# Performance work log

Hardware: AMD Instinct MI355X
Metric: run time of the kernel (lower is better)

## Reference

```python
import jax, jax.numpy as jnp
import numpy as np

B, T, V_ENC, V_DEC, E, H, A, MAX_SEQ = 32, 128, 32000, 32000, 512, 1024, 1024, 100


def setup_inputs() -> dict:
    key = jax.random.key(0)
    ks = jax.random.split(key, 16)
    s = 0.05
    p = lambda k, shape: jax.random.normal(k, shape, dtype=jnp.float32) * s
    inputs = jax.random.randint(ks[0], (B, T), 0, V_ENC, dtype=jnp.int32)
    return {
        'inputs': inputs,
        'enc_emb': p(ks[1], (V_ENC, E)),
        'enc_Wih': p(ks[2], (3 * H, E)),
        'enc_Whh': p(ks[3], (3 * H, H)),
        'enc_bih': p(ks[4], (3 * H,)),
        'enc_bhh': p(ks[5], (3 * H,)),
        'dec_emb': p(ks[6], (V_DEC, E)).at[0].set(0.0),  # padding_idx=0
        'dec_Wih': p(ks[7], (3 * H, E + A)),
        'dec_Whh': p(ks[8], (3 * H, H)),
        'dec_bih': p(ks[9], (3 * H,)),
        'dec_bhh': p(ks[10], (3 * H,)),
        'attn_W': p(ks[11], (A, 2 * H)),
        'attn_b': p(ks[12], (A,)),
        'cls_W': p(ks[13], (V_DEC, A)),
        'cls_b': p(ks[14], (V_DEC,)),
    }


def _gru_cell(x, h, Wih, Whh, bih, bhh):
    # PyTorch GRU cell math
    gi = x @ Wih.T + bih
    gh = h @ Whh.T + bhh
    i_r, i_z, i_n = jnp.split(gi, 3, axis=-1)
    h_r, h_z, h_n = jnp.split(gh, 3, axis=-1)
    r = jax.nn.sigmoid(i_r + h_r)
    z = jax.nn.sigmoid(i_z + h_z)
    n = jnp.tanh(i_n + r * h_n)
    return (1.0 - z) * n + z * h


def reference(inputs, enc_emb, enc_Wih, enc_Whh, enc_bih, enc_bhh,
              dec_emb, dec_Wih, dec_Whh, dec_bih, dec_bhh,
              attn_W, attn_b, cls_W, cls_b):
    b = inputs.shape[0]
    # ----- encoder -----
    emb = enc_emb[inputs]  # [B,T,E]
    def enc_step(h, x_t):
        h2 = _gru_cell(x_t, h, enc_Wih, enc_Whh, enc_bih, enc_bhh)
        return h2, h2
    h0 = jnp.zeros((b, H), emb.dtype)
    h_enc, enc_outputs = jax.lax.scan(enc_step, h0, emb.transpose(1, 0, 2))
    enc_outputs = enc_outputs.transpose(1, 0, 2)  # [B,T,H]

    # ----- greedy decoder, fixed max_sequence=100 steps -----
    def dec_step(carry, _):
        ids, attn_vec, h = carry
        x = jnp.concatenate([dec_emb[ids], attn_vec], axis=1)  # [B,E+A]
        h2 = _gru_cell(x, h, dec_Wih, dec_Whh, dec_bih, dec_bhh)  # [B,H]
        score = jnp.einsum('bth,bh->bt', enc_outputs, h2)
        w = jax.nn.softmax(score, axis=1)  # [B,T]
        context = jnp.einsum('bt,bth->bh', w, enc_outputs)  # [B,H]
        av = jnp.tanh(jnp.concatenate([context, h2], axis=1) @ attn_W.T + attn_b)  # [B,A]
        preds = av @ cls_W.T + cls_b  # [B,V]
        nids = jnp.argmax(preds, axis=1).astype(jnp.int32)
        return (nids, av, h2), (preds, w)

    carry0 = (jnp.zeros((b,), jnp.int32), jnp.zeros((b, A), jnp.float32), h_enc)
    _, (predictions, attn_weights) = jax.lax.scan(dec_step, carry0, None, length=MAX_SEQ)
    return predictions, attn_weights  # [100,B,V], [100,B,T]
```

## Files before the change

### kernel.cpp

```cpp
#include <hip/hip_runtime.h>
#include <hip/hip_cooperative_groups.h>
#include <math.h>

namespace cg = cooperative_groups;

#define NBLK 256
#define NTHR 1024
#define AG  __HIP_MEMORY_SCOPE_AGENT
#define SYS __HIP_MEMORY_SCOPE_SYSTEM

typedef float f4v __attribute__((ext_vector_type(4)));

constexpr int Bc = 32, Tc = 128, Ec = 512, Hc = 1024, Ac = 1024, Vc = 32000, Sc = 100;
constexpr long long OUT_ATTN = (long long)Sc * Bc * Vc;

constexpr long long O_ENCWIH = 0;
constexpr long long O_ENCWHH = O_ENCWIH + (long long)512 * 3072;
constexpr long long O_DECWIH = O_ENCWHH + (long long)1024 * 3072;
constexpr long long O_DECWHH = O_DECWIH + (long long)1536 * 3072;
constexpr long long O_ATTNWT = O_DECWHH + (long long)1024 * 3072;
constexpr long long O_CLSWT  = O_ATTNWT + (long long)2048 * 1024;
constexpr long long O_XENCT  = O_CLSWT + (long long)1024 * 32000;
constexpr long long O_GI     = O_XENCT + (long long)128 * 512 * 32;
constexpr long long O_ENCOUT = O_GI + (long long)128 * 32 * 3072;
constexpr long long O_H0     = O_ENCOUT + (long long)32 * 128 * 1024;
constexpr long long O_H1     = O_H0 + 32768;
constexpr long long O_H2     = O_H1 + 32768;
constexpr long long O_AVT    = O_H2 + 32768;
constexpr long long O_CTXT   = O_AVT + 32768;
constexpr long long O_PADEC  = O_CTXT + 32768;
constexpr long long O_PAENC  = O_PADEC + (long long)10 * 32 * 4096;
constexpr long long O_PAC    = O_PAENC + (long long)8 * 32 * 3072;
constexpr long long O_PARGV  = O_PAC + (long long)16 * 32 * 1024;
constexpr long long O_PARGI  = O_PARGV + 8000;
constexpr long long O_CNT    = O_PARGI + 8000;
constexpr long long WS_FLOATS = O_CNT + 1024;

#define CI_DA  0
#define CI_DB  32
#define CI_FIN 64
#define CI_DD  96
#define CI_H   128
#define CI_ENC 160
#define CI_DC  480

__device__ __forceinline__ float cohL(const float* p) { return __hip_atomic_load(p, __ATOMIC_RELAXED, SYS); }
__device__ __forceinline__ int   cohLi(const int* p) { return __hip_atomic_load(p, __ATOMIC_RELAXED, SYS); }

__device__ __forceinline__ void spinw(int* c, int tgt, int tid) {
  if (tid == 0) {
    while (__hip_atomic_load(c, __ATOMIC_RELAXED, AG) < tgt)
      __builtin_amdgcn_s_sleep(4);
  }
  __syncthreads();
}
__device__ __forceinline__ void sigp(int* c, int tid) {
  __syncthreads();
  if (tid == 0) {
    __builtin_amdgcn_fence(__ATOMIC_RELEASE, "agent");
    atomicAdd(c, 1);
  }
}

__global__ __launch_bounds__(NTHR, 4) void seq2seq_kernel(
    const int* __restrict__ inp, const float* __restrict__ encEmb,
    const float* __restrict__ encWih, const float* __restrict__ encWhh,
    const float* __restrict__ encBih, const float* __restrict__ encBhh,
    const float* __restrict__ decEmb, const float* __restrict__ decWih,
    const float* __restrict__ decWhh, const float* __restrict__ decBih,
    const float* __restrict__ decBhh, const float* __restrict__ attnW,
    const float* __restrict__ attnB, const float* __restrict__ clsW,
    const float* __restrict__ clsB, float* __restrict__ out,
    float* __restrict__ ws)
{
  cg::grid_group grid = cg::this_grid();
  const int bid = blockIdx.x, tid = threadIdx.x;
  const long long gtid = (long long)bid * NTHR + tid;
  int* cnt = (int*)(ws + O_CNT);

  __shared__ float smem[10624];
  int* sflag = (int*)(smem + 10600);
  int* nids  = (int*)(smem + 10368);

  {
    const int sg = tid >> 8, st = tid & 255;
    float* tile = smem + sg * 1056;
    const int c = st & 31, rr = st >> 5;
    for (int it = 0; it < 46; ++it) {
      int job = it * (NBLK * 4) + bid * 4 + sg;
      const float* src = nullptr; float* dst = nullptr;
      int R = 0, C = 0, tr = 0, tcd = 0;
      bool valid = true;
      int j = job;
      if (j < 1536)               { src = encWih; dst = ws + O_ENCWIH; R = 3072;  C = 512;  tr = j >> 4; tcd = j & 15; }
      else if ((j -= 1536) < 3072){ src = encWhh; dst = ws + O_ENCWHH; R = 3072;  C = 1024; tr = j >> 5; tcd = j & 31; }
      else if ((j -= 3072) < 4608){ src = decWih; dst = ws + O_DECWIH; R = 3072;  C = 1536; tr = j / 48; tcd = j % 48; }
      else if ((j -= 4608) < 3072){ src = decWhh; dst = ws + O_DECWHH; R = 3072;  C = 1024; tr = j >> 5; tcd = j & 31; }
      else if ((j -= 3072) < 2048){ src = attnW;  dst = ws + O_ATTNWT; R = 1024;  C = 2048; tr = j >> 6; tcd = j & 63; }
      else if ((j -= 2048) < 32000){src = clsW;   dst = ws + O_CLSWT;  R = 32000; C = 1024; tr = j >> 5; tcd = j & 31; }
      else valid = false;
      if (valid) {
        #pragma unroll
        for (int i = 0; i < 4; ++i) {
          int r = rr + (i << 3);
          tile[r * 33 + c] = src[(long long)(tr * 32 + r) * C + tcd * 32 + c];
        }
      }
      __syncthreads();
      if (valid) {
        #pragma unroll
        for (int i = 0; i < 4; ++i) {
          int c2 = rr + (i << 3);
          dst[(long long)(tcd * 32 + c2) * R + tr * 32 + c] = tile[c * 33 + c2];
        }
      }
      __syncthreads();
    }
  }
  for (long long i = gtid; i < (long long)128 * 512 * 32; i += (long long)NBLK * NTHR) {
    int b = (int)(i & 31);
    int k = (int)((i >> 5) & 511);
    int t = (int)(i >> 14);
    int row = inp[b * Tc + t];
    ws[O_XENCT + i] = encEmb[(long long)row * Ec + k];
  }
  for (long long i = gtid; i < 32768; i += (long long)NBLK * NTHR) {
    ws[O_H0 + i] = 0.f;
    ws[O_AVT + i] = 0.f;
  }
  grid.sync();

  for (int it = 0; it < 6; ++it) {
    int job = it * NBLK + bid;
    int t = job / 12, jc = job % 12;
    int jl = tid & 255, bq = tid >> 8;
    int j = jc * 256 + jl;
    float acc[8] = {0,0,0,0,0,0,0,0};
    const float* xb = ws + O_XENCT + (long long)t * 512 * 32 + bq * 8;
    const float* wb = ws + O_ENCWIH + j;
    for (int k = 0; k < 512; ++k) {
      float w = wb[(long long)k * 3072];
      float4 x0 = *(const float4*)(xb + k * 32);
      float4 x1 = *(const float4*)(xb + k * 32 + 4);
      acc[0] += x0.x * w; acc[1] += x0.y * w; acc[2] += x0.z * w; acc[3] += x0.w * w;
      acc[4] += x1.x * w; acc[5] += x1.y * w; acc[6] += x1.z * w; acc[7] += x1.w * w;
    }
    float bias = encBih[j];
    #pragma unroll
    for (int i = 0; i < 8; ++i) {
      int b = bq * 8 + i;
      __builtin_nontemporal_store(acc[i] + bias, &ws[O_GI + ((long long)t * 32 + b) * 3072 + j]);
    }
  }
  grid.sync();

  if (bid < 192) {
    int g = bid / 64, rem = bid % 64;
    int jc = rem >> 3, kp = rem & 7;
    for (int t = 0; t < Tc; ++t) {
      long long RD = (t & 1) ? O_H1 : O_H0;
      long long WR = (t & 1) ? O_H0 : O_H1;
      spinw(cnt + CI_H, 8 * t, tid);
      {
        const float* hsrc = ws + RD + kp * 4096;
        #pragma unroll
        for (int r = 0; r < 4; ++r)
          smem[r * 1024 + tid] = cohL(hsrc + r * 1024 + tid);
      }
      __syncthreads();
      int jl = tid & 127, bq = tid >> 7;
      int col = g * 1024 + jc * 128 + jl;
      int b0 = bq * 4;
      float acc[4] = {0,0,0,0};
      const float* hb = smem + b0;
      const float* wb = ws + O_ENCWHH + (long long)(kp * 128) * 3072 + col;
      for (int k = 0; k < 128; ++k) {
        float w = wb[(long long)k * 3072];
        float4 x = *(const float4*)(hb + k * 32);
        acc[0] += x.x * w; acc[1] += x.y * w; acc[2] += x.z * w; acc[3] += x.w * w;
      }
      #pragma unroll
      for (int i = 0; i < 4; ++i)
        ws[O_PAENC + ((long long)(kp * 32) + b0 + i) * 3072 + col] = acc[i];
      __syncthreads();
      if (tid == 0) {
        __builtin_amdgcn_fence(__ATOMIC_RELEASE, "agent");
        int old = atomicAdd(cnt + CI_ENC + jc * 32, 1);
        *sflag = (old == 24 * (t + 1) - 1) ? 1 : 0;
      }
      __syncthreads();
      if (*sflag) {
        int fj = tid & 127, fq = tid >> 7;
        int j = jc * 128 + fj;
        #pragma unroll
        for (int i = 0; i < 4; ++i) {
          int b = fq * 4 + i;
          float gr = 0, gz = 0, gn = 0;
          #pragma unroll
          for (int kp2 = 0; kp2 < 8; ++kp2) {
            long long base = O_PAENC + ((long long)(kp2 * 32) + b) * 3072;
            gr += cohL(&ws[base + j]);
            gz += cohL(&ws[base + 1024 + j]);
            gn += cohL(&ws[base + 2048 + j]);
          }
          long long gib = O_GI + ((long long)t * 32 + b) * 3072;
          float gir = ws[gib + j], giz = ws[gib + 1024 + j], gin = ws[gib + 2048 + j];
          float r = 1.f / (1.f + expf(-(gir + gr + encBhh[j])));
          float z = 1.f / (1.f + expf(-(giz + gz + encBhh[1024 + j])));
          float n = tanhf(gin + r * (gn + encBhh[2048 + j]));
          float hold = cohL(&ws[RD + (long long)j * 32 + b]);
          float hn = (1.f - z) * n + z * hold;
          ws[WR + (long long)j * 32 + b] = hn;
          ws[O_ENCOUT + ((long long)b * 128 + t) * 1024 + j] = hn;
          if (t == Tc - 1) ws[O_H2 + (long long)j * 32 + b] = hn;
        }
        sigp(cnt + CI_H, tid);
      }
      __syncthreads();
    }
  }

  for (int s = 0; s < Sc; ++s) {
    if (bid < 240) {
      int gate, loc;
      if (bid < 80)       { gate = 0; loc = bid; }
      else if (bid < 160) { gate = 1; loc = bid - 80; }
      else if (bid < 208) { gate = 2; loc = bid - 160; }
      else                { gate = 3; loc = bid - 208; }
      int nkp = (gate < 2) ? 10 : ((gate == 2) ? 6 : 4);
      int jc = loc / nkp, kp = loc % nkp;
      int kg = (gate == 3 ? 1536 : 0) + kp * 256;
      bool embp = (kg < 512);
      if (s == 0) {
        spinw(cnt + CI_H, 8 * Tc, tid);
        if (tid < 32) nids[tid] = 0;
        __syncthreads();
      } else if (embp) {
        spinw(cnt + CI_DD, 250 * s, tid);
        float* pv = smem; int* pi = (int*)(smem + 1024);
        int b = tid & 31, ch = tid >> 5;
        float bv = -3.4e38f; int bi = 0;
        for (int r = ch; r < 250; r += 32) {
          float v = cohL(&ws[O_PARGV + r * 32 + b]);
          int ix = cohLi(((int*)(ws + O_PARGI)) + r * 32 + b);
          if (v > bv || (v == bv && ix < bi)) { bv = v; bi = ix; }
        }
        pv[ch * 32 + b] = bv; pi[ch * 32 + b] = bi;
        __syncthreads();
        if (tid < 32) {
          float bb = -3.4e38f; int bbi = 0;
          for (int c2 = 0; c2 < 32; ++c2) {
            float v = pv[c2 * 32 + tid]; int ix = pi[c2 * 32 + tid];
            if (v > bb || (v == bb && ix < bbi)) { bb = v; bbi = ix; }
          }
          nids[tid] = bbi;
        }
        __syncthreads();
      } else {
        spinw(cnt + CI_DB, 32 * s, tid);
        spinw(cnt + CI_FIN, 16 * s, tid);
      }
      int jl = tid & 127, bq = tid >> 7;
      int b0 = bq * 4;
      int jcol = jc * 128 + jl;
      int wcol = (gate >= 2 ? 2048 : gate * 1024) + jcol;
      const float* wb = (kg < 1536) ? (ws + O_DECWIH + (long long)kg * 3072 + wcol)
                                    : (ws + O_DECWHH + (long long)(kg - 1536) * 3072 + wcol);
      float acc[4] = {0,0,0,0};
      if (embp) {
        const float* e0 = decEmb + (long long)nids[b0    ] * 512 + kg;
        const float* e1 = decEmb + (long long)nids[b0 + 1] * 512 + kg;
        const float* e2 = decEmb + (long long)nids[b0 + 2] * 512 + kg;
        const float* e3 = decEmb + (long long)nids[b0 + 3] * 512 + kg;
        for (int k = 0; k < 256; ++k) {
          float w = wb[(long long)k * 3072];
          acc[0] += e0[k] * w; acc[1] += e1[k] * w; acc[2] += e2[k] * w; acc[3] += e3[k] * w;
        }
      } else {
        const float* src = (kg < 1536) ? (ws + O_AVT + (long long)(kg - 512) * 32)
                                       : (ws + O_H2 + (long long)(kg - 1536) * 32);
        #pragma unroll
        for (int r = 0; r < 8; ++r)
          smem[r * 1024 + tid] = cohL(src + r * 1024 + tid);
        __syncthreads();
        const float* xb = smem + b0;
        for (int k = 0; k < 256; ++k) {
          float w = wb[(long long)k * 3072];
          float4 x = *(const float4*)(xb + k * 32);
          acc[0] += x.x * w; acc[1] += x.y * w; acc[2] += x.z * w; acc[3] += x.w * w;
        }
      }
      int colout = gate * 1024 + jcol;
      #pragma unroll
      for (int i = 0; i < 4; ++i)
        ws[O_PADEC + ((long long)(kp * 32) + b0 + i) * 4096 + colout] = acc[i];
      sigp(cnt + CI_DA, tid);
    }

    if (bid < 32) {
      spinw(cnt + CI_DA, 240 * (s + 1), tid);
      int b = bid;
      float* h2l = smem;
      float* scl = smem + 1024;
      float* wl  = smem + 1152;
      float* red = smem + 1280;
      {
        int j = tid;
        float gr = 0, gz = 0, gin = 0, ghn = 0;
        #pragma unroll
        for (int kp = 0; kp < 10; ++kp) {
          long long base = O_PADEC + ((long long)(kp * 32) + b) * 4096;
          gr += cohL(&ws[base + j]);
          gz += cohL(&ws[base + 1024 + j]);
          if (kp < 6) gin += cohL(&ws[base + 2048 + j]);
          if (kp < 4) ghn += cohL(&ws[base + 3072 + j]);
        }
        float r = 1.f / (1.f + expf(-(gr + decBih[j] + decBhh[j])));
        float z = 1.f / (1.f + expf(-(gz + decBih[1024 + j] + decBhh[1024 + j])));
        float n = tanhf(gin + decBih[2048 + j] + r * (ghn + decBhh[2048 + j]));
        float hold = ws[O_H2 + (long long)j * 32 + b];
        float h2 = (1.f - z) * n + z * hold;
        ws[O_H2 + (long long)j * 32 + b] = h2;
        h2l[j] = h2;
      }
      __syncthreads();
      {
        int wv = tid >> 6, lane = tid & 63;
        float h2v[16];
        #pragma unroll
        for (int i = 0; i < 16; ++i) h2v[i] = h2l[lane + (i << 6)];
        for (int t8 = 0; t8 < 8; ++t8) {
          int tt = wv * 8 + t8;
          const float* eo = ws + O_ENCOUT + ((long long)b * 128 + tt) * 1024 + lane;
          float a = 0;
          #pragma unroll
          for (int i = 0; i < 16; ++i) a += eo[i << 6] * h2v[i];
          #pragma unroll
          for (int off = 32; off; off >>= 1) a += __shfl_xor(a, off, 64);
          if (lane == 0) scl[tt] = a;
        }
      }
      __syncthreads();
      {
        float v = 0, m = -3.4e38f;
        if (tid < 128) {
          v = scl[tid]; m = v;
          #pragma unroll
          for (int off = 32; off; off >>= 1) m = fmaxf(m, __shfl_xor(m, off, 64));
          if ((tid & 63) == 0) red[tid >> 6] = m;
        }
        __syncthreads();
        float mm = fmaxf(red[0], red[1]);
        float e = 0.f;
        if (tid < 128) {
          e = expf(v - mm);
          float se = e;
          #pragma unroll
          for (int off = 32; off; off >>= 1) se += __shfl_xor(se, off, 64);
          if ((tid & 63) == 0) red[2 + (tid >> 6)] = se;
        }
        __syncthreads();
        if (tid < 128) {
          float wgt = e / (red[2] + red[3]);
          wl[tid] = wgt;
          __builtin_nontemporal_store(wgt, &out[OUT_ATTN + ((long long)s * 32 + b) * 128 + tid]);
        }
      }
      __syncthreads();
      {
        int j = tid;
        float a = 0;
        const float* eo = ws + O_ENCOUT + (long long)b * 128 * 1024 + j;
        for (int tt = 0; tt < 128; ++tt) a += wl[tt] * eo[(long long)tt * 1024];
        ws[O_CTXT + (long long)j * 32 + b] = a;
      }
      sigp(cnt + CI_DB, tid);
    }

    {
      spinw(cnt + CI_DB, 32 * (s + 1), tid);
      int jc = bid >> 4, kp = bid & 15;
      int kk0 = kp * 128;
      {
        const float* src = (kk0 < 1024) ? (ws + O_CTXT + (long long)kk0 * 32)
                                        : (ws + O_H2 + (long long)(kk0 - 1024) * 32);
        #pragma unroll
        for (int r = 0; r < 4; ++r)
          smem[r * 1024 + tid] = cohL(src + r * 1024 + tid);
      }
      __syncthreads();
      int jl = tid & 63, bh = tid >> 6;
      int b0 = bh * 2;
      int j = jc * 64 + jl;
      float acc0 = 0, acc1 = 0;
      const float* wb = ws + O_ATTNWT + (long long)kk0 * 1024 + j;
      const float* xb = smem + b0;
      for (int k = 0; k < 128; ++k) {
        float w = wb[(long long)k * 1024];
        float2 x = *(const float2*)(xb + k * 32);
        acc0 += x.x * w; acc1 += x.y * w;
      }
      ws[O_PAC + ((long long)(kp * 32) + b0) * 1024 + j] = acc0;
      ws[O_PAC + ((long long)(kp * 32) + b0 + 1) * 1024 + j] = acc1;
      __syncthreads();
      if (tid == 0) {
        __builtin_amdgcn_fence(__ATOMIC_RELEASE, "agent");
        int old = atomicAdd(cnt + CI_DC + jc * 32, 1);
        *sflag = (old == 16 * (s + 1) - 1) ? 1 : 0;
      }
      __syncthreads();
      if (*sflag) {
        #pragma unroll
        for (int o = 0; o < 2; ++o) {
          int oo = tid + o * 1024;
          int j2 = jc * 64 + (oo >> 5), b = oo & 31;
          float sum = 0;
          #pragma unroll
          for (int kp2 = 0; kp2 < 16; ++kp2)
            sum += cohL(&ws[O_PAC + ((long long)(kp2 * 32) + b) * 1024 + j2]);
          ws[O_AVT + (long long)j2 * 32 + b] = tanhf(sum + attnB[j2]);
        }
        sigp(cnt + CI_FIN, tid);
      }
      __syncthreads();
    }

    if (bid < 250) {
      spinw(cnt + CI_FIN, 16 * (s + 1), tid);
      float* wc  = smem;
      float* sav = smem + 8192;
      int jl = tid & 127, bg = tid >> 7;
      int b0 = bg * 4;
      int j = bid * 128 + jl;
      float acc[4] = {0,0,0,0};
      for (int kc = 0; kc < 1024; kc += 64) {
        #pragma unroll
        for (int i = 0; i < 2; ++i) {
          int t4 = tid + i * 1024;
          int kk = t4 >> 5, c4 = t4 & 31;
          f4v wv = __builtin_nontemporal_load(
            (const f4v*)(ws + O_CLSWT + (long long)(kc + kk) * 32000 + bid * 128 + c4 * 4));
          *(f4v*)(wc + kk * 128 + c4 * 4) = wv;
        }
        #pragma unroll
        for (int i = 0; i < 2; ++i)
          sav[i * 1024 + tid] = cohL(ws + O_AVT + (long long)kc * 32 + i * 1024 + tid);
        __syncthreads();
        for (int k = 0; k < 64; ++k) {
          float w = wc[k * 128 + jl];
          float4 a = *(const float4*)(sav + k * 32 + b0);
          acc[0] += a.x * w; acc[1] += a.y * w; acc[2] += a.z * w; acc[3] += a.w * w;
        }
        __syncthreads();
      }
      float cb = clsB[j];
      float pvv[4];
      #pragma unroll
      for (int i = 0; i < 4; ++i) {
        pvv[i] = acc[i] + cb;
        __builtin_nontemporal_store(pvv[i], &out[((long long)s * 32 + b0 + i) * 32000 + j]);
      }
      float* lv = smem;
      int*   li = (int*)(smem + 4096);
      __syncthreads();
      #pragma unroll
      for (int i = 0; i < 4; ++i) {
        lv[(b0 + i) * 128 + jl] = pvv[i];
        li[(b0 + i) * 128 + jl] = j;
      }
      __syncthreads();
      float* l2v = smem + 8192;
      int*   l2i = (int*)(smem + 9216);
      {
        int b = tid >> 5, r = tid & 31;
        float bv = -3.4e38f; int bi2 = 0;
        #pragma unroll
        for (int i = 0; i < 4; ++i) {
          float v = lv[b * 128 + r + (i << 5)];
          int ix = li[b * 128 + r + (i << 5)];
          if (v > bv || (v == bv && ix < bi2)) { bv = v; bi2 = ix; }
        }
        l2v[b * 32 + r] = bv; l2i[b * 32 + r] = bi2;
      }
      __syncthreads();
      if (tid < 32) {
        float bv = -3.4e38f; int bi2 = 0;
        for (int r = 0; r < 32; ++r) {
          float v = l2v[tid * 32 + r]; int ix = l2i[tid * 32 + r];
          if (v > bv || (v == bv && ix < bi2)) { bv = v; bi2 = ix; }
        }
        ws[O_PARGV + bid * 32 + tid] = bv;
        ((int*)(ws + O_PARGI))[bid * 32 + tid] = bi2;
      }
      sigp(cnt + CI_DD, tid);
    }
  }
}

extern "C" void kernel_launch(void* const* d_in, const int* in_sizes, int n_in,
                              void* d_out, int out_size, void* d_ws, size_t ws_size,
                              hipStream_t stream) {
  const int*   inp    = (const int*)  d_in[0];
  const float* encEmb = (const float*)d_in[1];
  const float* encWih = (const float*)d_in[2];
  const float* encWhh = (const float*)d_in[3];
  const float* encBih = (const float*)d_in[4];
  const float* encBhh = (const float*)d_in[5];
  const float* decEmb = (const float*)d_in[6];
  const float* decWih = (const float*)d_in[7];
  const float* decWhh = (const float*)d_in[8];
  const float* decBih = (const float*)d_in[9];
  const float* decBhh = (const float*)d_in[10];
  const float* attnW  = (const float*)d_in[11];
  const float* attnB  = (const float*)d_in[12];
  const float* clsW   = (const float*)d_in[13];
  const float* clsB   = (const float*)d_in[14];
  float* out = (float*)d_out;
  float* ws  = (float*)d_ws;

  if (ws_size < (size_t)WS_FLOATS * sizeof(float)) return;

  (void)hipMemsetAsync(ws + O_CNT, 0, 1024 * sizeof(int), stream);

  void* args[] = { &inp, &encEmb, &encWih, &encWhh, &encBih, &encBhh,
                   &decEmb, &decWih, &decWhh, &decBih, &decBhh,
                   &attnW, &attnB, &clsW, &clsB, &out, &ws };
  (void)hipLaunchCooperativeKernel((void*)seq2seq_kernel, dim3(NBLK), dim3(NTHR),
                                   args, 0, stream);
}
```

Baseline: 46.03 ms.

## Replace atomic counters with per-block flag slots and restructure attention projection

Swaps the shared atomic counters used for inter-stage barriers in the decoder loop for per-block flag slots holding step tags. Waiters poll many slots in parallel, one thread per producer, which removes atomic contention on a single counter. The attention output projection moves from a 256-block split-K with partial sums and last-arriver reduction to 32 blocks that each compute full dot products, dropping one sync round and the partial buffer at the cost of less parallelism. The class-weight loads also become ordinary loads instead of nontemporal ones.

```diff
diff --git a/kernel.cpp b/kernel.cpp
--- a/kernel.cpp
+++ b/kernel.cpp
@@ -30,19 +30,19 @@
 constexpr long long O_CTXT   = O_AVT + 32768;
 constexpr long long O_PADEC  = O_CTXT + 32768;
 constexpr long long O_PAENC  = O_PADEC + (long long)10 * 32 * 4096;
-constexpr long long O_PAC    = O_PAENC + (long long)8 * 32 * 3072;
-constexpr long long O_PARGV  = O_PAC + (long long)16 * 32 * 1024;
+constexpr long long O_PARGV  = O_PAENC + (long long)8 * 32 * 3072;
 constexpr long long O_PARGI  = O_PARGV + 8000;
 constexpr long long O_CNT    = O_PARGI + 8000;
-constexpr long long WS_FLOATS = O_CNT + 1024;
-
-#define CI_DA  0
-#define CI_DB  32
-#define CI_FIN 64
-#define CI_DD  96
+constexpr long long O_SLOT   = O_CNT + 1024;
+constexpr long long WS_FLOATS = O_SLOT + 1024;
+
 #define CI_H   128
 #define CI_ENC 160
-#define CI_DC  480
+
+#define SL_DA  0
+#define SL_DB  256
+#define SL_FIN 320
+#define SL_DD  384
 
 __device__ __forceinline__ float cohL(const float* p) { return __hip_atomic_load(p, __ATOMIC_RELAXED, SYS); }
 __device__ __forceinline__ int   cohLi(const int* p) { return __hip_atomic_load(p, __ATOMIC_RELAXED, SYS); }
@@ -60,6 +60,21 @@
     __builtin_amdgcn_fence(__ATOMIC_RELEASE, "agent");
     atomicAdd(c, 1);
   }
+}
+
+__device__ __forceinline__ void sigs(int* slotp, int tag, int tid) {
+  __syncthreads();
+  if (tid == 0) {
+    __builtin_amdgcn_fence(__ATOMIC_RELEASE, "agent");
+    __hip_atomic_store(slotp, tag, __ATOMIC_RELAXED, AG);
+  }
+}
+__device__ __forceinline__ void pollN(const int* slots, int n, int tag, int tid) {
+  if (tid < n) {
+    while (__hip_atomic_load(&slots[tid], __ATOMIC_RELAXED, AG) < tag)
+      __builtin_amdgcn_s_sleep(2);
+  }
+  __syncthreads();
 }
 
 __global__ __launch_bounds__(NTHR, 4) void seq2seq_kernel(
@@ -76,7 +91,8 @@
   cg::grid_group grid = cg::this_grid();
   const int bid = blockIdx.x, tid = threadIdx.x;
   const long long gtid = (long long)bid * NTHR + tid;
-  int* cnt = (int*)(ws + O_CNT);
+  int* cnt  = (int*)(ws + O_CNT);
+  int* slot = (int*)(ws + O_SLOT);
 
   __shared__ float smem[10624];
   int* sflag = (int*)(smem + 10600);
@@ -236,7 +252,7 @@
         if (tid < 32) nids[tid] = 0;
         __syncthreads();
       } else if (embp) {
-        spinw(cnt + CI_DD, 250 * s, tid);
+        pollN(slot + SL_DD, 250, s, tid);
         float* pv = smem; int* pi = (int*)(smem + 1024);
         int b = tid & 31, ch = tid >> 5;
         float bv = -3.4e38f; int bi = 0;
@@ -256,9 +272,10 @@
           nids[tid] = bbi;
         }
         __syncthreads();
+      } else if (kg >= 1536) {
+        pollN(slot + SL_DB, 32, s, tid);
       } else {
-        spinw(cnt + CI_DB, 32 * s, tid);
-        spinw(cnt + CI_FIN, 16 * s, tid);
+        pollN(slot + SL_FIN, 32, s, tid);
       }
       int jl = tid & 127, bq = tid >> 7;
       int b0 = bq * 4;
@@ -294,11 +311,11 @@
       #pragma unroll
       for (int i = 0; i < 4; ++i)
         ws[O_PADEC + ((long long)(kp * 32) + b0 + i) * 4096 + colout] = acc[i];
-      sigp(cnt + CI_DA, tid);
+      sigs(slot + SL_DA + bid, s + 1, tid);
     }
 
     if (bid < 32) {
-      spinw(cnt + CI_DA, 240 * (s + 1), tid);
+      pollN(slot + SL_DA, 240, s + 1, tid);
       int b = bid;
       float* h2l = smem;
       float* scl = smem + 1024;
@@ -374,59 +391,36 @@
         for (int tt = 0; tt < 128; ++tt) a += wl[tt] * eo[(long long)tt * 1024];
         ws[O_CTXT + (long long)j * 32 + b] = a;
       }
-      sigp(cnt + CI_DB, tid);
-    }
-
-    {
-      spinw(cnt + CI_DB, 32 * (s + 1), tid);
-      int jc = bid >> 4, kp = bid & 15;
-      int kk0 = kp * 128;
-      {
+      sigs(slot + SL_DB + bid, s + 1, tid);
+    }
+
+    if (bid < 32) {
+      pollN(slot + SL_DB, 32, s + 1, tid);
+      int jf = tid >> 5, b = tid & 31;
+      int j = (bid << 5) + jf;
+      float sum = 0.f;
+      #pragma unroll 1
+      for (int kp = 0; kp < 16; ++kp) {
+        int kk0 = kp * 128;
         const float* src = (kk0 < 1024) ? (ws + O_CTXT + (long long)kk0 * 32)
                                         : (ws + O_H2 + (long long)(kk0 - 1024) * 32);
         #pragma unroll
         for (int r = 0; r < 4; ++r)
           smem[r * 1024 + tid] = cohL(src + r * 1024 + tid);
-      }
-      __syncthreads();
-      int jl = tid & 63, bh = tid >> 6;
-      int b0 = bh * 2;
-      int j = jc * 64 + jl;
-      float acc0 = 0, acc1 = 0;
-      const float* wb = ws + O_ATTNWT + (long long)kk0 * 1024 + j;
-      const float* xb = smem + b0;
-      for (int k = 0; k < 128; ++k) {
-        float w = wb[(long long)k * 1024];
-        float2 x = *(const float2*)(xb + k * 32);
-        acc0 += x.x * w; acc1 += x.y * w;
-      }
-      ws[O_PAC + ((long long)(kp * 32) + b0) * 1024 + j] = acc0;
-      ws[O_PAC + ((long long)(kp * 32) + b0 + 1) * 1024 + j] = acc1;
-      __syncthreads();
-      if (tid == 0) {
-        __builtin_amdgcn_fence(__ATOMIC_RELEASE, "agent");
-        int old = atomicAdd(cnt + CI_DC + jc * 32, 1);
-        *sflag = (old == 16 * (s + 1) - 1) ? 1 : 0;
-      }
-      __syncthreads();
-      if (*sflag) {
-        #pragma unroll
-        for (int o = 0; o < 2; ++o) {
-          int oo = tid + o * 1024;
-          int j2 = jc * 64 + (oo >> 5), b = oo & 31;
-          float sum = 0;
-          #pragma unroll
-          for (int kp2 = 0; kp2 < 16; ++kp2)
-            sum += cohL(&ws[O_PAC + ((long long)(kp2 * 32) + b) * 1024 + j2]);
-          ws[O_AVT + (long long)j2 * 32 + b] = tanhf(sum + attnB[j2]);
-        }
-        sigp(cnt + CI_FIN, tid);
-      }
-      __syncthreads();
+        __syncthreads();
+        const float* wk = ws + O_ATTNWT + (long long)kk0 * 1024 + j;
+        float pp = 0.f;
+        for (int k = 0; k < 128; ++k)
+          pp += smem[k * 32 + b] * wk[(long long)k * 1024];
+        sum += pp;
+        __syncthreads();
+      }
+      ws[O_AVT + (long long)j * 32 + b] = tanhf(sum + attnB[j]);
+      sigs(slot + SL_FIN + bid, s + 1, tid);
     }
 
     if (bid < 250) {
-      spinw(cnt + CI_FIN, 16 * (s + 1), tid);
+      pollN(slot + SL_FIN, 32, s + 1, tid);
       float* wc  = smem;
       float* sav = smem + 8192;
       int jl = tid & 127, bg = tid >> 7;
@@ -438,9 +432,8 @@
         for (int i = 0; i < 2; ++i) {
           int t4 = tid + i * 1024;
           int kk = t4 >> 5, c4 = t4 & 31;
-          f4v wv = __builtin_nontemporal_load(
-            (const f4v*)(ws + O_CLSWT + (long long)(kc + kk) * 32000 + bid * 128 + c4 * 4));
-          *(f4v*)(wc + kk * 128 + c4 * 4) = wv;
+          *(f4v*)(wc + kk * 128 + c4 * 4) =
+            *(const f4v*)(ws + O_CLSWT + (long long)(kc + kk) * 32000 + bid * 128 + c4 * 4);
         }
         #pragma unroll
         for (int i = 0; i < 2; ++i)
@@ -492,7 +485,7 @@
         ws[O_PARGV + bid * 32 + tid] = bv;
         ((int*)(ws + O_PARGI))[bid * 32 + tid] = bi2;
       }
-      sigp(cnt + CI_DD, tid);
+      sigs(slot + SL_DD + bid, s + 1, tid);
     }
   }
 }
@@ -520,7 +513,7 @@
 
   if (ws_size < (size_t)WS_FLOATS * sizeof(float)) return;
 
-  (void)hipMemsetAsync(ws + O_CNT, 0, 1024 * sizeof(int), stream);
+  (void)hipMemsetAsync(ws + O_CNT, 0, 2048 * sizeof(int), stream);
 
   void* args[] = { &inp, &encEmb, &encWih, &encWhh, &encBih, &encBhh,
                    &decEmb, &decWih, &decWhh, &decBih, &decBhh,
```

New measurement: 116.3 ms. 153% more time.
